# Kernel optimization log

Measured on AMD Instinct MI355X. Metric: run time of the kernel, lower is better.

Reference implementation:

```python
import jax, jax.numpy as jnp
import numpy as np

N_NODES = 50000
N_EDGES = 800000
IN_FEAT = 256
OUT_FEAT = 128
P_EDGE = 0.2   # edge dropout rate
P_NODE = 0.1   # node-feature dropout rate
BN_EPS = 1e-5


def setup_inputs() -> dict:
    key = jax.random.key(0)
    ks = jax.random.split(key, 8)
    features = jax.random.normal(ks[0], (N_NODES, IN_FEAT), dtype=jnp.float32)
    W = jax.random.normal(ks[1], (IN_FEAT, OUT_FEAT), dtype=jnp.float32) / np.sqrt(IN_FEAT)
    b = jnp.zeros((OUT_FEAT,), dtype=jnp.float32)
    gamma = jnp.ones((OUT_FEAT,), dtype=jnp.float32)
    beta = jnp.zeros((OUT_FEAT,), dtype=jnp.float32)
    src = jax.random.randint(ks[2], (N_EDGES,), 0, N_NODES, dtype=jnp.int64)
    dst = jax.random.randint(ks[3], (N_EDGES,), 0, N_NODES, dtype=jnp.int64)
    edge_rand = jax.random.uniform(ks[4], (N_EDGES,), dtype=jnp.float32)
    node_rand = jax.random.uniform(ks[5], (N_NODES, OUT_FEAT), dtype=jnp.float32)
    return {"features": features, "W": W, "b": b, "gamma": gamma, "beta": beta,
            "src": src, "dst": dst, "edge_rand": edge_rand, "node_rand": node_rand}


def reference(features, W, b, gamma, beta, src, dst, edge_rand, node_rand):
    dt = features.dtype
    # --- edge dropout: keep-mask over edges (no rescale, per DropEdge convention) ---
    emask = (edge_rand >= P_EDGE).astype(dt)                      # [E]
    # --- GCN conv, norm='both' on the dropped graph ---
    h = features @ W                                              # [N, out] (W first: out < in)
    deg_src = jax.ops.segment_sum(emask, src, num_segments=N_NODES)  # out-degrees
    deg_dst = jax.ops.segment_sum(emask, dst, num_segments=N_NODES)  # in-degrees
    coef = emask * jax.lax.rsqrt(jnp.maximum(deg_src[src], 1.0) * jnp.maximum(deg_dst[dst], 1.0))
    msg = h[src] * coef[:, None]                                  # [E, out]
    agg = jax.ops.segment_sum(msg, dst, num_segments=N_NODES) + b  # [N, out]
    # --- BatchNorm1d (training mode: batch statistics over nodes) ---
    mean = jnp.mean(agg, axis=0)
    var = jnp.var(agg, axis=0)
    y = (agg - mean) * jax.lax.rsqrt(var + BN_EPS) * gamma + beta
    # --- node-feature dropout (inverted scaling) ---
    nmask = (node_rand >= P_NODE).astype(dt) / (1.0 - P_NODE)
    return y * nmask
```

## Files before the change

kernel.cpp:

```cpp
#include <hip/hip_runtime.h>

#define N_NODES 50000
#define N_EDGES 800000
#define IN_FEAT 256
#define OUT_FEAT 128
#define P_EDGE 0.2f
#define P_NODE 0.1f
#define BN_EPS 1e-5f
#define CAP 64
#define GEMM_BLOCKS 782
#define EDGE_BLOCKS 782
#define ZERO_BLOCKS 98
#define PREPW_BLOCKS 128
#define AGG_BLOCKS 2048
#define FIN_BLOCKS 8

typedef __bf16 bf16x8 __attribute__((ext_vector_type(8)));
typedef float floatx4 __attribute__((ext_vector_type(4)));
typedef float f32x4 __attribute__((ext_vector_type(4)));
typedef int i32x4 __attribute__((ext_vector_type(4)));

__device__ inline float bflo(unsigned u) { return __uint_as_float(u << 16); }
__device__ inline float bfhi(unsigned u) { return __uint_as_float(u & 0xffff0000u); }

__global__ __launch_bounds__(256) void k_init(const float* __restrict__ W,
    uint4* __restrict__ zero_base, __bf16* __restrict__ Wt) {
  if (blockIdx.x < ZERO_BLOCKS) {
    int i = blockIdx.x * 256 + threadIdx.x;
    if (i < 25000) zero_base[i] = make_uint4(0u, 0u, 0u, 0u);
  } else {
    int idx = (blockIdx.x - ZERO_BLOCKS) * 256 + threadIdx.x;
    int k = idx >> 7, n = idx & 127;
    Wt[n * IN_FEAT + k] = (__bf16)W[idx];
  }
}

__device__ inline bf16x8 cvt8(f32x4 a, f32x4 b) {
  bf16x8 v;
  v[0] = (__bf16)a[0]; v[1] = (__bf16)a[1]; v[2] = (__bf16)a[2]; v[3] = (__bf16)a[3];
  v[4] = (__bf16)b[0]; v[5] = (__bf16)b[1]; v[6] = (__bf16)b[2]; v[7] = (__bf16)b[3];
  return v;
}

__device__ void gemm_body(int bid, const float* __restrict__ feat,
    const __bf16* __restrict__ Wt, __bf16* __restrict__ h) {
  const int lane = threadIdx.x & 63;
  const int wave = threadIdx.x >> 6;
  const int l16 = lane & 15;
  const int quad = lane >> 4;
  const int m0 = bid * 64 + wave * 16;

  int mload = m0 + l16;
  if (mload >= N_NODES) mload = N_NODES - 1;

  bf16x8 a[8];
#pragma unroll
  for (int kk = 0; kk < 8; kk++) {
    const f32x4* p = (const f32x4*)(feat + (size_t)mload * IN_FEAT + kk * 32 + quad * 8);
    f32x4 f0 = __builtin_nontemporal_load(p);
    f32x4 f1 = __builtin_nontemporal_load(p + 1);
    a[kk] = cvt8(f0, f1);
  }

  floatx4 acc[8];
#pragma unroll
  for (int g = 0; g < 8; g++) {
    const __bf16* wrow = Wt + (size_t)(g * 16 + l16) * IN_FEAT + quad * 8;
    floatx4 c = {0.f, 0.f, 0.f, 0.f};
#pragma unroll
    for (int kk = 0; kk < 8; kk++) {
      bf16x8 b = *(const bf16x8*)(wrow + kk * 32);
      c = __builtin_amdgcn_mfma_f32_16x16x32_bf16(a[kk], b, c, 0, 0, 0);
    }
    acc[g] = c;
  }

  const int rbase = m0 + quad * 4;
#pragma unroll
  for (int g = 0; g < 8; g++) {
#pragma unroll
    for (int r = 0; r < 4; r++) {
      int row = rbase + r;
      if (row < N_NODES)
        h[(size_t)row * OUT_FEAT + g * 16 + l16] = (__bf16)acc[g][r];
    }
  }
}

__global__ __launch_bounds__(256) void k_fused(const float* __restrict__ feat,
    const __bf16* __restrict__ Wt, __bf16* __restrict__ h,
    const int* __restrict__ src, const int* __restrict__ dst,
    const float* __restrict__ er, unsigned* __restrict__ deg_src,
    unsigned* __restrict__ deg_dst, unsigned short* __restrict__ edge_src) {
  if (blockIdx.x < GEMM_BLOCKS) {
    gemm_body(blockIdx.x, feat, Wt, h);
  } else {
    int t = (blockIdx.x - GEMM_BLOCKS) * 256 + threadIdx.x;
    if (t < N_EDGES / 4) {
      f32x4 e4 = __builtin_nontemporal_load((const f32x4*)er + t);
      i32x4 s4 = __builtin_nontemporal_load((const i32x4*)src + t);
      i32x4 d4 = __builtin_nontemporal_load((const i32x4*)dst + t);
      const bool k0 = e4[0] >= P_EDGE, k1 = e4[1] >= P_EDGE;
      const bool k2 = e4[2] >= P_EDGE, k3 = e4[3] >= P_EDGE;
      if (k0) atomicAdd(&deg_src[s4[0]], 1u);
      if (k1) atomicAdd(&deg_src[s4[1]], 1u);
      if (k2) atomicAdd(&deg_src[s4[2]], 1u);
      if (k3) atomicAdd(&deg_src[s4[3]], 1u);
      unsigned p0 = 0xffffffffu, p1 = 0xffffffffu, p2 = 0xffffffffu, p3 = 0xffffffffu;
      if (k0) p0 = atomicAdd(&deg_dst[d4[0]], 1u);
      if (k1) p1 = atomicAdd(&deg_dst[d4[1]], 1u);
      if (k2) p2 = atomicAdd(&deg_dst[d4[2]], 1u);
      if (k3) p3 = atomicAdd(&deg_dst[d4[3]], 1u);
      if (p0 < CAP) edge_src[(unsigned)d4[0] * CAP + p0] = (unsigned short)s4[0];
      if (p1 < CAP) edge_src[(unsigned)d4[1] * CAP + p1] = (unsigned short)s4[1];
      if (p2 < CAP) edge_src[(unsigned)d4[2] * CAP + p2] = (unsigned short)s4[2];
      if (p3 < CAP) edge_src[(unsigned)d4[3] * CAP + p3] = (unsigned short)s4[3];
    }
  }
}

__global__ __launch_bounds__(256) void k_agg(const unsigned short* __restrict__ h,
    const unsigned short* __restrict__ edge_src, const unsigned* __restrict__ deg_src,
    const unsigned* __restrict__ deg_dst, const float* __restrict__ bias,
    float* __restrict__ out, float* __restrict__ psum, float* __restrict__ pssq) {
  const int wid = threadIdx.x >> 6;
  const int lane = threadIdx.x & 63;
  const int g = lane >> 4;
  const int cl = lane & 15;
  const int wave_global = blockIdx.x * 4 + wid;

  float b8[8];
#pragma unroll
  for (int j = 0; j < 8; j++) b8[j] = bias[cl * 8 + j];

  float s8[8], ss8[8];
#pragma unroll
  for (int j = 0; j < 8; j++) { s8[j] = 0.f; ss8[j] = 0.f; }

  for (int d = wave_global; d < N_NODES; d += AGG_BLOCKS * 4) {
    const unsigned cnt = deg_dst[d];
    unsigned lim = cnt > CAP ? CAP : cnt;
    const unsigned base = (unsigned)d * CAP;
    float acc[8];
#pragma unroll
    for (int j = 0; j < 8; j++) acc[j] = 0.f;

#pragma unroll 2
    for (unsigned i = 0; i < lim; i += 4) {
      unsigned e = i + (unsigned)g;
      bool valid = e < lim;
      unsigned idx = (unsigned)edge_src[base + (valid ? e : 0u)];
      unsigned dg = deg_src[idx];
      float r = valid ? rsqrtf((float)(dg ? dg : 1u)) : 0.f;
      uint4 u = *(const uint4*)(h + (size_t)idx * OUT_FEAT + cl * 8);
      acc[0] = fmaf(bflo(u.x), r, acc[0]);
      acc[1] = fmaf(bfhi(u.x), r, acc[1]);
      acc[2] = fmaf(bflo(u.y), r, acc[2]);
      acc[3] = fmaf(bfhi(u.y), r, acc[3]);
      acc[4] = fmaf(bflo(u.z), r, acc[4]);
      acc[5] = fmaf(bfhi(u.z), r, acc[5]);
      acc[6] = fmaf(bflo(u.w), r, acc[6]);
      acc[7] = fmaf(bfhi(u.w), r, acc[7]);
    }
#pragma unroll
    for (int j = 0; j < 8; j++) {
      acc[j] += __shfl_xor(acc[j], 16);
      acc[j] += __shfl_xor(acc[j], 32);
    }
    if (g == 0) {
      float sc = rsqrtf((float)(cnt ? cnt : 1u));
      float o[8];
#pragma unroll
      for (int j = 0; j < 8; j++) {
        o[j] = fmaf(acc[j], sc, b8[j]);
        s8[j] += o[j];
        ss8[j] = fmaf(o[j], o[j], ss8[j]);
      }
      float4 o0 = make_float4(o[0], o[1], o[2], o[3]);
      float4 o1 = make_float4(o[4], o[5], o[6], o[7]);
      *(float4*)(out + (size_t)d * OUT_FEAT + cl * 8) = o0;
      *(float4*)(out + (size_t)d * OUT_FEAT + cl * 8 + 4) = o1;
    }
  }

  __shared__ float ls[4][16][8], lss[4][16][8];
  if (g == 0) {
#pragma unroll
    for (int j = 0; j < 8; j++) { ls[wid][cl][j] = s8[j]; lss[wid][cl][j] = ss8[j]; }
  }
  __syncthreads();
  if (threadIdx.x < 128) {
    int pcl = threadIdx.x >> 3, pj = threadIdx.x & 7;
    float t = ls[0][pcl][pj] + ls[1][pcl][pj] + ls[2][pcl][pj] + ls[3][pcl][pj];
    float t2 = lss[0][pcl][pj] + lss[1][pcl][pj] + lss[2][pcl][pj] + lss[3][pcl][pj];
    psum[blockIdx.x * OUT_FEAT + threadIdx.x] = t;
    pssq[blockIdx.x * OUT_FEAT + threadIdx.x] = t2;
  }
}

__global__ __launch_bounds__(256) void k_fin(const float* __restrict__ psum,
    const float* __restrict__ pssq, const float* __restrict__ gamma,
    const float* __restrict__ beta, float* __restrict__ a_coef,
    float* __restrict__ b_coef) {
  const int col16 = threadIdx.x & 15;
  const int slice = threadIdx.x >> 4;
  const int c = blockIdx.x * 16 + col16;
  float t = 0.f, t2 = 0.f;
  for (int b = slice; b < AGG_BLOCKS; b += 16) {
    t += psum[b * OUT_FEAT + c];
    t2 += pssq[b * OUT_FEAT + c];
  }
  __shared__ float S[16][17], S2[16][17];
  S[slice][col16] = t;
  S2[slice][col16] = t2;
  __syncthreads();
  if (threadIdx.x < 16) {
    float ts = 0.f, tss = 0.f;
#pragma unroll
    for (int s = 0; s < 16; s++) { ts += S[s][threadIdx.x]; tss += S2[s][threadIdx.x]; }
    int cc = blockIdx.x * 16 + threadIdx.x;
    float mean = ts * (1.0f / N_NODES);
    float var = tss * (1.0f / N_NODES) - mean * mean;
    float a = gamma[cc] * rsqrtf(var + BN_EPS);
    a_coef[cc] = a;
    b_coef[cc] = fmaf(-mean, a, beta[cc]);
  }
}

__global__ __launch_bounds__(256) void k_norm(float* __restrict__ out,
    const float* __restrict__ node_rand, const float* __restrict__ a_coef,
    const float* __restrict__ b_coef) {
  const size_t total4 = (size_t)N_NODES * OUT_FEAT / 4;
  size_t i = (size_t)blockIdx.x * 256 + threadIdx.x;
  if (i < total4) {
    int c0 = (int)((i * 4) & 127);
    f32x4 v = ((const f32x4*)out)[i];
    f32x4 nr = __builtin_nontemporal_load((const f32x4*)node_rand + i);
    f32x4 a = *(const f32x4*)(a_coef + c0);
    f32x4 b = *(const f32x4*)(b_coef + c0);
    const float inv = 1.0f / (1.0f - P_NODE);
    f32x4 o;
    o[0] = (nr[0] >= P_NODE ? inv : 0.f) * fmaf(v[0], a[0], b[0]);
    o[1] = (nr[1] >= P_NODE ? inv : 0.f) * fmaf(v[1], a[1], b[1]);
    o[2] = (nr[2] >= P_NODE ? inv : 0.f) * fmaf(v[2], a[2], b[2]);
    o[3] = (nr[3] >= P_NODE ? inv : 0.f) * fmaf(v[3], a[3], b[3]);
    __builtin_nontemporal_store(o, (f32x4*)out + i);
  }
}

extern "C" void kernel_launch(void* const* d_in, const int* in_sizes, int n_in,
                              void* d_out, int out_size, void* d_ws, size_t ws_size,
                              hipStream_t stream) {
  const float* feat  = (const float*)d_in[0];
  const float* W     = (const float*)d_in[1];
  const float* bias  = (const float*)d_in[2];
  const float* gamma = (const float*)d_in[3];
  const float* beta  = (const float*)d_in[4];
  const int*   src   = (const int*)d_in[5];
  const int*   dst   = (const int*)d_in[6];
  const float* er    = (const float*)d_in[7];
  const float* nr    = (const float*)d_in[8];
  float* out = (float*)d_out;

  char* ws = (char*)d_ws;
  __bf16*         h        = (__bf16*)        (ws + 0);
  unsigned short* edge_src = (unsigned short*)(ws + 12800000);
  __bf16*         Wt       = (__bf16*)        (ws + 19200000);
  unsigned*       deg_src  = (unsigned*)      (ws + 19265536);
  unsigned*       deg_dst  = (unsigned*)      (ws + 19465536);
  float*          psum     = (float*)         (ws + 19665536);
  float*          pssq     = (float*)         (ws + 20714112);
  float*          a_coef   = (float*)         (ws + 21762688);
  float*          b_coef   = (float*)         (ws + 21763200);

  k_init<<<ZERO_BLOCKS + PREPW_BLOCKS, 256, 0, stream>>>(
      W, (uint4*)(ws + 19265536), Wt);
  k_fused<<<GEMM_BLOCKS + EDGE_BLOCKS, 256, 0, stream>>>(
      feat, Wt, h, src, dst, er, deg_src, deg_dst, edge_src);
  k_agg<<<AGG_BLOCKS, 256, 0, stream>>>((const unsigned short*)h, edge_src,
      deg_src, deg_dst, bias, out, psum, pssq);
  k_fin<<<FIN_BLOCKS, 256, 0, stream>>>(psum, pssq, gamma, beta, a_coef, b_coef);
  k_norm<<<(N_NODES * OUT_FEAT / 4 + 255) / 256, 256, 0, stream>>>(out, nr, a_coef, b_coef);
}
```

Before: 290.2 us.

## Split edge/GEMM kernels, stage W in swizzled LDS, coalesce h stores

Splits the fused GEMM+edge kernel into two separate launches. The GEMM now stages the bf16 W into 64KB of XOR-swizzled LDS and restages output tiles through LDS so h is written with coalesced 16-byte row stores. It also halves the aggregation grid, raises the aggregation unroll factor, drops the nontemporal hints in the normalise kernel, and moves the psum/pssq workspace offsets. The split removes the overlap between the atomic-bound edge pass and the GEMM, and the 64KB LDS per block limits GEMM occupancy.

```diff
diff --git a/kernel.cpp b/kernel.cpp
--- a/kernel.cpp
+++ b/kernel.cpp
@@ -12,7 +12,7 @@
 #define EDGE_BLOCKS 782
 #define ZERO_BLOCKS 98
 #define PREPW_BLOCKS 128
-#define AGG_BLOCKS 2048
+#define AGG_BLOCKS 1024
 #define FIN_BLOCKS 8
 
 typedef __bf16 bf16x8 __attribute__((ext_vector_type(8)));
@@ -42,80 +42,98 @@
   return v;
 }
 
-__device__ void gemm_body(int bid, const float* __restrict__ feat,
-    const __bf16* __restrict__ Wt, __bf16* __restrict__ h) {
-  const int lane = threadIdx.x & 63;
-  const int wave = threadIdx.x >> 6;
-  const int l16 = lane & 15;
-  const int quad = lane >> 4;
-  const int m0 = bid * 64 + wave * 16;
-
-  int mload = m0 + l16;
-  if (mload >= N_NODES) mload = N_NODES - 1;
-
-  bf16x8 a[8];
-#pragma unroll
-  for (int kk = 0; kk < 8; kk++) {
-    const f32x4* p = (const f32x4*)(feat + (size_t)mload * IN_FEAT + kk * 32 + quad * 8);
-    f32x4 f0 = __builtin_nontemporal_load(p);
-    f32x4 f1 = __builtin_nontemporal_load(p + 1);
-    a[kk] = cvt8(f0, f1);
-  }
-
-  floatx4 acc[8];
-#pragma unroll
-  for (int g = 0; g < 8; g++) {
-    const __bf16* wrow = Wt + (size_t)(g * 16 + l16) * IN_FEAT + quad * 8;
-    floatx4 c = {0.f, 0.f, 0.f, 0.f};
-#pragma unroll
-    for (int kk = 0; kk < 8; kk++) {
-      bf16x8 b = *(const bf16x8*)(wrow + kk * 32);
-      c = __builtin_amdgcn_mfma_f32_16x16x32_bf16(a[kk], b, c, 0, 0, 0);
-    }
-    acc[g] = c;
-  }
-
-  const int rbase = m0 + quad * 4;
-#pragma unroll
-  for (int g = 0; g < 8; g++) {
-#pragma unroll
-    for (int r = 0; r < 4; r++) {
-      int row = rbase + r;
-      if (row < N_NODES)
-        h[(size_t)row * OUT_FEAT + g * 16 + l16] = (__bf16)acc[g][r];
-    }
-  }
-}
-
-__global__ __launch_bounds__(256) void k_fused(const float* __restrict__ feat,
-    const __bf16* __restrict__ Wt, __bf16* __restrict__ h,
+__global__ __launch_bounds__(256) void k_edge(
     const int* __restrict__ src, const int* __restrict__ dst,
     const float* __restrict__ er, unsigned* __restrict__ deg_src,
     unsigned* __restrict__ deg_dst, unsigned short* __restrict__ edge_src) {
-  if (blockIdx.x < GEMM_BLOCKS) {
-    gemm_body(blockIdx.x, feat, Wt, h);
-  } else {
-    int t = (blockIdx.x - GEMM_BLOCKS) * 256 + threadIdx.x;
-    if (t < N_EDGES / 4) {
-      f32x4 e4 = __builtin_nontemporal_load((const f32x4*)er + t);
-      i32x4 s4 = __builtin_nontemporal_load((const i32x4*)src + t);
-      i32x4 d4 = __builtin_nontemporal_load((const i32x4*)dst + t);
-      const bool k0 = e4[0] >= P_EDGE, k1 = e4[1] >= P_EDGE;
-      const bool k2 = e4[2] >= P_EDGE, k3 = e4[3] >= P_EDGE;
-      if (k0) atomicAdd(&deg_src[s4[0]], 1u);
-      if (k1) atomicAdd(&deg_src[s4[1]], 1u);
-      if (k2) atomicAdd(&deg_src[s4[2]], 1u);
-      if (k3) atomicAdd(&deg_src[s4[3]], 1u);
-      unsigned p0 = 0xffffffffu, p1 = 0xffffffffu, p2 = 0xffffffffu, p3 = 0xffffffffu;
-      if (k0) p0 = atomicAdd(&deg_dst[d4[0]], 1u);
-      if (k1) p1 = atomicAdd(&deg_dst[d4[1]], 1u);
-      if (k2) p2 = atomicAdd(&deg_dst[d4[2]], 1u);
-      if (k3) p3 = atomicAdd(&deg_dst[d4[3]], 1u);
-      if (p0 < CAP) edge_src[(unsigned)d4[0] * CAP + p0] = (unsigned short)s4[0];
-      if (p1 < CAP) edge_src[(unsigned)d4[1] * CAP + p1] = (unsigned short)s4[1];
-      if (p2 < CAP) edge_src[(unsigned)d4[2] * CAP + p2] = (unsigned short)s4[2];
-      if (p3 < CAP) edge_src[(unsigned)d4[3] * CAP + p3] = (unsigned short)s4[3];
-    }
+  int t = blockIdx.x * 256 + threadIdx.x;
+  if (t < N_EDGES / 4) {
+    f32x4 e4 = ((const f32x4*)er)[t];
+    i32x4 s4 = ((const i32x4*)src)[t];
+    i32x4 d4 = ((const i32x4*)dst)[t];
+    const bool k0 = e4[0] >= P_EDGE, k1 = e4[1] >= P_EDGE;
+    const bool k2 = e4[2] >= P_EDGE, k3 = e4[3] >= P_EDGE;
+    if (k0) atomicAdd(&deg_src[s4[0]], 1u);
+    if (k1) atomicAdd(&deg_src[s4[1]], 1u);
+    if (k2) atomicAdd(&deg_src[s4[2]], 1u);
+    if (k3) atomicAdd(&deg_src[s4[3]], 1u);
+    unsigned p0 = 0xffffffffu, p1 = 0xffffffffu, p2 = 0xffffffffu, p3 = 0xffffffffu;
+    if (k0) p0 = atomicAdd(&deg_dst[d4[0]], 1u);
+    if (k1) p1 = atomicAdd(&deg_dst[d4[1]], 1u);
+    if (k2) p2 = atomicAdd(&deg_dst[d4[2]], 1u);
+    if (k3) p3 = atomicAdd(&deg_dst[d4[3]], 1u);
+    if (p0 < CAP) edge_src[(unsigned)d4[0] * CAP + p0] = (unsigned short)s4[0];
+    if (p1 < CAP) edge_src[(unsigned)d4[1] * CAP + p1] = (unsigned short)s4[1];
+    if (p2 < CAP) edge_src[(unsigned)d4[2] * CAP + p2] = (unsigned short)s4[2];
+    if (p3 < CAP) edge_src[(unsigned)d4[3] * CAP + p3] = (unsigned short)s4[3];
+  }
+}
+
+__global__ __launch_bounds__(256, 2) void k_gemm(const float* __restrict__ feat,
+    const __bf16* __restrict__ Wt, __bf16* __restrict__ h) {
+  __shared__ char lds[65536];
+  const int t = threadIdx.x;
+
+  const uint4* wsrc = (const uint4*)Wt;
+#pragma unroll
+  for (int i = 0; i < 16; i++) {
+    int c = i * 256 + t;
+    unsigned o = (unsigned)c * 16u;
+    unsigned row = o >> 9;
+    *(uint4*)(lds + (o ^ ((row & 7u) << 4))) = wsrc[c];
+  }
+  __syncthreads();
+
+  const int lane = t & 63;
+  const int wave = t >> 6;
+  const int l16 = lane & 15;
+  const int quad = lane >> 4;
+  const int m0 = blockIdx.x * 64 + wave * 16;
+
+  int mload = m0 + l16;
+  if (mload >= N_NODES) mload = N_NODES - 1;
+
+  bf16x8 a[8];
+#pragma unroll
+  for (int kk = 0; kk < 8; kk++) {
+    const f32x4* p = (const f32x4*)(feat + (size_t)mload * IN_FEAT + kk * 32 + quad * 8);
+    a[kk] = cvt8(p[0], p[1]);
+  }
+
+  floatx4 acc[8];
+#pragma unroll
+  for (int g = 0; g < 8; g++) {
+    const unsigned row = (unsigned)(g * 16 + l16);
+    const unsigned base = row * 512u + (unsigned)quad * 16u;
+    const unsigned swz = (row & 7u) << 4;
+    floatx4 c = {0.f, 0.f, 0.f, 0.f};
+#pragma unroll
+    for (int kk = 0; kk < 8; kk++) {
+      bf16x8 b = *(const bf16x8*)(lds + ((base + (unsigned)kk * 64u) ^ swz));
+      c = __builtin_amdgcn_mfma_f32_16x16x32_bf16(a[kk], b, c, 0, 0, 0);
+    }
+    acc[g] = c;
+  }
+  __syncthreads();
+
+  char* hb = lds + wave * 16384;
+#pragma unroll
+  for (int g = 0; g < 8; g++) {
+#pragma unroll
+    for (int r = 0; r < 4; r++) {
+      unsigned row = (unsigned)(quad * 4 + r);
+      unsigned o = row * 256u + (unsigned)(g * 16 + l16) * 2u;
+      *(__bf16*)(hb + (o ^ ((row & 7u) << 4))) = (__bf16)acc[g][r];
+    }
+  }
+#pragma unroll
+  for (int j = 0; j < 4; j++) {
+    unsigned row = (unsigned)(lane >> 4) + (unsigned)j * 4u;
+    unsigned o = row * 256u + (unsigned)(lane & 15) * 16u;
+    uint4 v = *(const uint4*)(hb + (o ^ ((row & 7u) << 4)));
+    int grow = m0 + (int)row;
+    if (grow < N_NODES)
+      *(uint4*)((char*)h + (size_t)grow * 256 + (size_t)(lane & 15) * 16) = v;
   }
 }
 
@@ -145,7 +163,7 @@
 #pragma unroll
     for (int j = 0; j < 8; j++) acc[j] = 0.f;
 
-#pragma unroll 2
+#pragma unroll 4
     for (unsigned i = 0; i < lim; i += 4) {
       unsigned e = i + (unsigned)g;
       bool valid = e < lim;
@@ -235,7 +253,7 @@
   if (i < total4) {
     int c0 = (int)((i * 4) & 127);
     f32x4 v = ((const f32x4*)out)[i];
-    f32x4 nr = __builtin_nontemporal_load((const f32x4*)node_rand + i);
+    f32x4 nr = ((const f32x4*)node_rand)[i];
     f32x4 a = *(const f32x4*)(a_coef + c0);
     f32x4 b = *(const f32x4*)(b_coef + c0);
     const float inv = 1.0f / (1.0f - P_NODE);
@@ -244,7 +262,7 @@
     o[1] = (nr[1] >= P_NODE ? inv : 0.f) * fmaf(v[1], a[1], b[1]);
     o[2] = (nr[2] >= P_NODE ? inv : 0.f) * fmaf(v[2], a[2], b[2]);
     o[3] = (nr[3] >= P_NODE ? inv : 0.f) * fmaf(v[3], a[3], b[3]);
-    __builtin_nontemporal_store(o, (f32x4*)out + i);
+    ((f32x4*)out)[i] = o;
   }
 }
 
@@ -269,14 +287,14 @@
   unsigned*       deg_src  = (unsigned*)      (ws + 19265536);
   unsigned*       deg_dst  = (unsigned*)      (ws + 19465536);
   float*          psum     = (float*)         (ws + 19665536);
-  float*          pssq     = (float*)         (ws + 20714112);
-  float*          a_coef   = (float*)         (ws + 21762688);
-  float*          b_coef   = (float*)         (ws + 21763200);
+  float*          pssq     = (float*)         (ws + 20189824);
+  float*          a_coef   = (float*)         (ws + 20714112);
+  float*          b_coef   = (float*)         (ws + 20714624);
 
   k_init<<<ZERO_BLOCKS + PREPW_BLOCKS, 256, 0, stream>>>(
       W, (uint4*)(ws + 19265536), Wt);
-  k_fused<<<GEMM_BLOCKS + EDGE_BLOCKS, 256, 0, stream>>>(
-      feat, Wt, h, src, dst, er, deg_src, deg_dst, edge_src);
+  k_edge<<<EDGE_BLOCKS, 256, 0, stream>>>(src, dst, er, deg_src, deg_dst, edge_src);
+  k_gemm<<<GEMM_BLOCKS, 256, 0, stream>>>(feat, Wt, h);
   k_agg<<<AGG_BLOCKS, 256, 0, stream>>>((const unsigned short*)h, edge_src,
       deg_src, deg_dst, bias, out, psum, pssq);
   k_fin<<<FIN_BLOCKS, 256, 0, stream>>>(psum, pssq, gamma, beta, a_coef, b_coef);
```

Measured after the change: 282.7 us. 1.03x faster.
